# Kernel optimization log

Measured on AMD Instinct MI355X. Metric: run time of the kernel, lower is better.

Reference implementation:

```python
import jax, jax.numpy as jnp
import numpy as np

N = 50000      # nodes
E = 400000     # edges (avg degree 8)
G = 64         # graphs in batch
IN_DIM = 128
OUT_DIM = 16


def _linear_params(key, fan_in, fan_out):
    k1, k2 = jax.random.split(key)
    s = 1.0 / np.sqrt(fan_in)
    W = jax.random.uniform(k1, (fan_in, fan_out), minval=-s, maxval=s, dtype=jnp.float32)
    b = jax.random.uniform(k2, (fan_out,), minval=-s, maxval=s, dtype=jnp.float32)
    return W, b


def setup_inputs() -> dict:
    key = jax.random.key(0)
    ks = jax.random.split(key, 12)
    x = jax.random.normal(ks[0], (N, IN_DIM), dtype=jnp.float32)
    edge_index = jax.random.randint(ks[1], (2, E), 0, N)
    # balanced graph assignment (sorted, every graph id present)
    batch = (jnp.arange(N) * G) // N
    W1, b1 = _linear_params(ks[2], IN_DIM, 64)
    W2, b2 = _linear_params(ks[3], 64, 256)
    W3, b3 = _linear_params(ks[4], 256, 512)
    W4, b4 = _linear_params(ks[5], 512, 64)
    Wr, br = _linear_params(ks[6], IN_DIM, 64)
    fc1_W, fc1_b = _linear_params(ks[7], 64, 64)
    fc2_W, fc2_b = _linear_params(ks[8], 64, OUT_DIM)
    ln_g = jnp.ones((64,), jnp.float32); ln_b = jnp.zeros((64,), jnp.float32)
    fcn_g = jnp.ones((64,), jnp.float32); fcn_b = jnp.zeros((64,), jnp.float32)
    return dict(x=x, edge_index=edge_index, batch=batch,
                W1=W1, b1=b1, W2=W2, b2=b2, W3=W3, b3=b3, W4=W4, b4=b4,
                Wr=Wr, br=br, ln_g=ln_g, ln_b=ln_b,
                fc1_W=fc1_W, fc1_b=fc1_b, fcn_g=fcn_g, fcn_b=fcn_b,
                fc2_W=fc2_W, fc2_b=fc2_b)


def _leaky_relu(h):
    return jnp.where(h >= 0, h, 0.01 * h)


def _layer_norm(h, g, b, eps=1e-5):
    m = jnp.mean(h, axis=-1, keepdims=True)
    v = jnp.var(h, axis=-1, keepdims=True)
    return (h - m) * jax.lax.rsqrt(v + eps) * g + b


def reference(x, edge_index, batch, W1, b1, W2, b2, W3, b3, W4, b4,
              Wr, br, ln_g, ln_b, fc1_W, fc1_b, fcn_g, fcn_b, fc2_W, fc2_b):
    src, dst = edge_index[0], edge_index[1]
    n = x.shape[0]
    # PyG GCNConv normalization with self-loops: deg = 1 + in-degree
    deg = jax.ops.segment_sum(jnp.ones(src.shape[0], x.dtype), dst, num_segments=n) + 1.0
    dis = jax.lax.rsqrt(deg)                 # [N]
    edge_norm = (dis[src] * dis[dst])[:, None]   # [E,1]
    self_norm = (dis * dis)[:, None]             # [N,1]

    def gcn_conv(h, W, b):
        h = h @ W                                            # transform first (PyG order)
        agg = jax.ops.segment_sum(h[src] * edge_norm, dst, num_segments=n)
        return agg + h * self_norm + b                       # self-loop term + bias

    residual = x @ Wr + br
    h = _leaky_relu(gcn_conv(x, W1, b1))
    h = _leaky_relu(gcn_conv(h, W2, b2))
    h = _leaky_relu(gcn_conv(h, W3, b3))
    h = _leaky_relu(gcn_conv(h, W4, b4))
    h = _layer_norm(h + residual, ln_g, ln_b)
    # global max pool over graphs
    p = jax.ops.segment_max(h, batch, num_segments=G)        # [G,64]
    p = _layer_norm(p @ fc1_W + fc1_b, fcn_g, fcn_b)
    p = _leaky_relu(p)
    return p @ fc2_W + fc2_b                                 # [G,16]
```

## Files before the change

kernel.cpp:

```cpp
#include <hip/hip_runtime.h>
#include <hip/hip_bf16.h>
#include <math.h>

typedef short bf16x8 __attribute__((ext_vector_type(8)));
typedef short bf16x4 __attribute__((ext_vector_type(4)));
typedef float f32x4 __attribute__((ext_vector_type(4)));

__device__ inline unsigned short f2bf(float f) {
  unsigned u = __float_as_uint(f);
  u += 0x7FFF + ((u >> 16) & 1);
  return (unsigned short)(u >> 16);
}
__device__ inline float bf2f(unsigned short h) {
  return __uint_as_float(((unsigned)h) << 16);
}


__global__ __launch_bounds__(256) void zero_i32(int* __restrict__ p, int n) {
  int i = blockIdx.x * 256 + threadIdx.x;
  if (i < n) p[i] = 0;
}

__global__ __launch_bounds__(256) void count_k(const int* __restrict__ dst, int* __restrict__ cnt, int e) {
  int i = blockIdx.x * 256 + threadIdx.x;
  if (i < e) atomicAdd(&cnt[dst[i]], 1);
}

__global__ __launch_bounds__(256) void dis_k(const int* __restrict__ cnt, float* __restrict__ dis, int n) {
  int i = blockIdx.x * 256 + threadIdx.x;
  if (i < n) dis[i] = rsqrtf((float)cnt[i] + 1.0f);
}

__global__ __launch_bounds__(256) void scan_a(const int* __restrict__ cnt, int* __restrict__ bsum, int n) {
  int i = blockIdx.x * 256 + threadIdx.x;
  int v = (i < n) ? cnt[i] : 0;
#pragma unroll
  for (int o = 32; o > 0; o >>= 1) v += __shfl_xor(v, o);
  __shared__ int ws[4];
  if ((threadIdx.x & 63) == 0) ws[threadIdx.x >> 6] = v;
  __syncthreads();
  if (threadIdx.x == 0) bsum[blockIdx.x] = ws[0] + ws[1] + ws[2] + ws[3];
}

__global__ __launch_bounds__(256) void scan_b(const int* __restrict__ bsum, int* __restrict__ bpre,
                                              int* __restrict__ off_n, int nb) {
  __shared__ int s[256];
  int t = threadIdx.x;
  int v = (t < nb) ? bsum[t] : 0;
  s[t] = v;
  __syncthreads();
  for (int o = 1; o < 256; o <<= 1) {
    int u = (t >= o) ? s[t - o] : 0;
    __syncthreads();
    s[t] += u;
    __syncthreads();
  }
  if (t < nb) bpre[t] = s[t] - v;
  if (t == 255) off_n[0] = s[255];
}

__global__ __launch_bounds__(256) void scan_c(const int* __restrict__ cnt, const int* __restrict__ bpre,
                                              int* __restrict__ off, int* __restrict__ cursor, int n) {
  __shared__ int s[256];
  int i = blockIdx.x * 256 + threadIdx.x;
  int t = threadIdx.x;
  int v = (i < n) ? cnt[i] : 0;
  s[t] = v;
  __syncthreads();
  for (int o = 1; o < 256; o <<= 1) {
    int u = (t >= o) ? s[t - o] : 0;
    __syncthreads();
    s[t] += u;
    __syncthreads();
  }
  if (i < n) {
    int ov = bpre[blockIdx.x] + s[t] - v;
    off[i] = ov;
    cursor[i] = ov;
  }
}

__global__ __launch_bounds__(256) void scatter_k(const int* __restrict__ src, const int* __restrict__ dst,
                                                 int* __restrict__ cursor, int* __restrict__ csr, int e) {
  int i = blockIdx.x * 256 + threadIdx.x;
  if (i < e) {
    int p = atomicAdd(&cursor[dst[i]], 1);
    csr[p] = src[i];
  }
}


__global__ __launch_bounds__(256) void wconv_k(const float* __restrict__ W1, const float* __restrict__ Wr,
                                               const float* __restrict__ W2, const float* __restrict__ W3,
                                               const float* __restrict__ W4,
                                               short* __restrict__ o1, short* __restrict__ oR,
                                               short* __restrict__ o2, short* __restrict__ o3,
                                               short* __restrict__ o4) {
  int b = blockIdx.x;
  const float* W; short* O; int K, N, nr;
  if (b < 64)       { W = W1; O = o1; K = 128; N = 64;  nr = b; }
  else if (b < 128) { W = Wr; O = oR; K = 128; N = 64;  nr = b - 64; }
  else if (b < 384) { W = W2; O = o2; K = 64;  N = 256; nr = b - 128; }
  else if (b < 896) { W = W3; O = o3; K = 256; N = 512; nr = b - 384; }
  else              { W = W4; O = o4; K = 512; N = 64;  nr = b - 896; }
  for (int k = threadIdx.x; k < K; k += 256)
    O[(size_t)nr * K + k] = (short)f2bf(W[(size_t)k * N + nr]);
}


template<int KT, int NTOT, int WM, int WN, int BIAS, int RELU, int ABF, int OBF, int SPLIT, int SCL, int BLK>
__global__ __launch_bounds__(256, BLK) void mgemm(const void* __restrict__ Av,
                                                  const short* __restrict__ Wc,
                                                  const float* __restrict__ bias,
                                                  void* __restrict__ Cv, void* __restrict__ Cv2,
                                                  const float* __restrict__ scl, int M) {
  __shared__ short As[64 * WM][ABF ? 40 : 72];
  __shared__ short Bs[64 * WN][40];
  const int tid = threadIdx.x;
  const int row0 = blockIdx.x * (64 * WM);
  const int col0 = blockIdx.y * (64 * WN);
  const int w = tid >> 6, lane = tid & 63;
  const int wm = w / WN, wn = w % WN;
  const int rm = wm * 64, cn = wn * 64;
  const int lm = lane & 15, lk = (lane >> 4) * 8;

  f32x4 acc[4][4];
#pragma unroll
  for (int i = 0; i < 4; i++)
#pragma unroll
    for (int j = 0; j < 4; j++)
#pragma unroll
      for (int r = 0; r < 4; r++) acc[i][j][r] = 0.f;

  for (int k0 = 0; k0 < KT; k0 += 32) {
#pragma unroll
    for (int p = 0; p < WM; p++) {
      int r = (tid >> 2) + p * 64;
      int kseg = (tid & 3) * 8;
      int gr = row0 + r;
      if (ABF) {
        bf16x8 v = {0, 0, 0, 0, 0, 0, 0, 0};
        if (gr < M) v = *(const bf16x8*)((const short*)Av + (size_t)gr * KT + k0 + kseg);
        *(bf16x8*)&As[r][kseg] = v;
      } else {
        float4 v0 = {0.f, 0.f, 0.f, 0.f}, v1 = {0.f, 0.f, 0.f, 0.f};
        if (gr < M) {
          const float* ap = (const float*)Av + (size_t)gr * KT + k0 + kseg;
          v0 = *(const float4*)ap;
          v1 = *(const float4*)(ap + 4);
        }
        float vv[8] = {v0.x, v0.y, v0.z, v0.w, v1.x, v1.y, v1.z, v1.w};
        bf16x8 hv, lv;
#pragma unroll
        for (int j = 0; j < 8; j++) {
          unsigned short h = f2bf(vv[j]);
          hv[j] = (short)h;
          lv[j] = (short)f2bf(vv[j] - bf2f(h));
        }
        *(bf16x8*)&As[r][kseg] = hv;
        *(bf16x8*)&As[r][32 + kseg] = lv;
      }
    }
#pragma unroll
    for (int p = 0; p < WN; p++) {
      int nr = (tid >> 2) + p * 64;
      int seg = (tid & 3) * 8;
      *(bf16x8*)&Bs[nr][seg] = *(const bf16x8*)(Wc + (size_t)(col0 + nr) * KT + k0 + seg);
    }
    __syncthreads();

    bf16x8 ah[4], al[4], bb[4];
#pragma unroll
    for (int mt = 0; mt < 4; mt++) {
      ah[mt] = *(const bf16x8*)&As[rm + mt * 16 + lm][lk];
      if (!ABF) al[mt] = *(const bf16x8*)&As[rm + mt * 16 + lm][32 + lk];
    }
#pragma unroll
    for (int nt = 0; nt < 4; nt++) bb[nt] = *(const bf16x8*)&Bs[cn + nt * 16 + lm][lk];
#pragma unroll
    for (int mt = 0; mt < 4; mt++)
#pragma unroll
      for (int nt = 0; nt < 4; nt++) {
        acc[mt][nt] = __builtin_amdgcn_mfma_f32_16x16x32_bf16(ah[mt], bb[nt], acc[mt][nt], 0, 0, 0);
        if (!ABF)
          acc[mt][nt] = __builtin_amdgcn_mfma_f32_16x16x32_bf16(al[mt], bb[nt], acc[mt][nt], 0, 0, 0);
      }
    __syncthreads();
  }

  if (SPLIT) {
    float* O = (wn == 0) ? (float*)Cv : (float*)Cv2;
#pragma unroll
    for (int mt = 0; mt < 4; mt++) {
      int grb = row0 + rm + mt * 16 + (lane >> 4) * 4;
#pragma unroll
      for (int nt = 0; nt < 4; nt++) {
        int gc = nt * 16 + lm;
        float bv = (wn == 1) ? bias[gc] : 0.f;
#pragma unroll
        for (int r = 0; r < 4; r++) {
          int gr = grb + r;
          if (gr < M) {
            float v = acc[mt][nt][r];
            if (wn == 0 && SCL) v *= scl[gr];
            else v += bv;
            O[(size_t)gr * 64 + gc] = v;
          }
        }
      }
    }
  } else if (OBF && WM == 1) {
    short* epi = &Bs[0][0];
    const int NCOL = 64 * WN;
    float bvv[4];
#pragma unroll
    for (int nt = 0; nt < 4; nt++) bvv[nt] = BIAS ? bias[col0 + cn + nt * 16 + lm] : 0.f;
#pragma unroll
    for (int mt = 0; mt < 4; mt++) {
      __syncthreads();
#pragma unroll
      for (int r = 0; r < 4; r++) {
        int gr = row0 + mt * 16 + (lane >> 4) * 4 + r;
        float sc = (SCL && gr < M) ? scl[gr] : 1.f;
#pragma unroll
        for (int nt = 0; nt < 4; nt++) {
          float v = acc[mt][nt][r] + bvv[nt];
          if (RELU) v = (v >= 0.f) ? v : 0.01f * v;
          if (SCL) v *= sc;
          epi[((lane >> 4) * 4 + r) * NCOL + cn + nt * 16 + lm] = (short)f2bf(v);
        }
      }
      __syncthreads();
      const int per = (16 * NCOL) / 256;
      int base = tid * per;
      int lr = base / NCOL, lc = base % NCOL;
      int gr = row0 + mt * 16 + lr;
      if (gr < M) {
#pragma unroll
        for (int q = 0; q < per / 8; q++)
          *(bf16x8*)((short*)Cv + (size_t)gr * NTOT + col0 + lc + q * 8) = *(bf16x8*)&epi[base + q * 8];
      }
    }
  } else {
#pragma unroll
    for (int mt = 0; mt < 4; mt++) {
      int grb = row0 + rm + mt * 16 + (lane >> 4) * 4;
#pragma unroll
      for (int nt = 0; nt < 4; nt++) {
        int gc = col0 + cn + nt * 16 + lm;
        float bv = BIAS ? bias[gc] : 0.f;
#pragma unroll
        for (int r = 0; r < 4; r++) {
          int gr = grb + r;
          if (gr < M) {
            float v = acc[mt][nt][r] + bv;
            if (RELU) v = (v >= 0.f) ? v : 0.01f * v;
            if (SCL) v *= scl[gr];
            if (OBF) ((short*)Cv)[(size_t)gr * NTOT + gc] = (short)f2bf(v);
            else     ((float*)Cv)[(size_t)gr * NTOT + gc] = v;
          }
        }
      }
    }
  }
}


__global__ __launch_bounds__(256, 3) void fused34_k(const short* __restrict__ z3,
                                                    const short* __restrict__ W3c,
                                                    const float* __restrict__ b3,
                                                    const short* __restrict__ W4c,
                                                    const float* __restrict__ dis,
                                                    float* __restrict__ T4, int M) {
  __shared__ short Bs[64][264];
  __shared__ short Hs[64][72];
  __shared__ short Ws4[64][72];
  const int tid = threadIdx.x;
  const int row0 = blockIdx.x * 64;
  const int w = tid >> 6, lane = tid & 63;
  const int lm = lane & 15, lk = (lane >> 4) * 8;
  const int rquad = (lane >> 4) * 4;
  const int srow = tid >> 2, sseg = (tid & 3) * 8;

  bf16x8 afr[8];
  {
    int gr = row0 + w * 16 + lm;
    bool ok = gr < M;
    const short* zp = z3 + (size_t)gr * 256 + lk;
#pragma unroll
    for (int kc = 0; kc < 8; kc++) {
      bf16x8 v = {0, 0, 0, 0, 0, 0, 0, 0};
      if (ok) v = *(const bf16x8*)(zp + kc * 32);
      afr[kc] = v;
    }
  }

  f32x4 t4acc[4];
#pragma unroll
  for (int nt = 0; nt < 4; nt++)
#pragma unroll
    for (int r = 0; r < 4; r++) t4acc[nt][r] = 0.f;

  for (int c = 0; c < 8; c++) {
#pragma unroll
    for (int q = 0; q < 8; q++) {
      int flat = q * 2048 + tid * 8;
      int rr = flat >> 8, cc = flat & 255;
      *(bf16x8*)&Bs[rr][cc] = *(const bf16x8*)(W3c + (size_t)c * 64 * 256 + flat);
    }
    *(bf16x8*)&Ws4[srow][sseg]      = *(const bf16x8*)(W4c + (size_t)srow * 512 + c * 64 + sseg);
    *(bf16x8*)&Ws4[srow][32 + sseg] = *(const bf16x8*)(W4c + (size_t)srow * 512 + c * 64 + 32 + sseg);
    __syncthreads();

    f32x4 acc1[4];
#pragma unroll
    for (int nt = 0; nt < 4; nt++)
#pragma unroll
      for (int r = 0; r < 4; r++) acc1[nt][r] = 0.f;
#pragma unroll
    for (int k0 = 0; k0 < 8; k0++) {
      bf16x8 bb[4];
#pragma unroll
      for (int nt = 0; nt < 4; nt++) bb[nt] = *(const bf16x8*)&Bs[nt * 16 + lm][k0 * 32 + lk];
#pragma unroll
      for (int nt = 0; nt < 4; nt++)
        acc1[nt] = __builtin_amdgcn_mfma_f32_16x16x32_bf16(afr[k0], bb[nt], acc1[nt], 0, 0, 0);
    }
#pragma unroll
    for (int nt = 0; nt < 4; nt++) {
      float bv = b3[c * 64 + nt * 16 + lm];
#pragma unroll
      for (int r = 0; r < 4; r++) {
        float v = acc1[nt][r] + bv;
        v = (v >= 0.f) ? v : 0.01f * v;
        Hs[w * 16 + rquad + r][nt * 16 + lm] = (short)f2bf(v);
      }
    }
#pragma unroll
    for (int kk = 0; kk < 64; kk += 32) {
      bf16x8 ah2 = *(const bf16x8*)&Hs[w * 16 + lm][kk + lk];
      bf16x8 bb2[4];
#pragma unroll
      for (int nt = 0; nt < 4; nt++) bb2[nt] = *(const bf16x8*)&Ws4[nt * 16 + lm][kk + lk];
#pragma unroll
      for (int nt = 0; nt < 4; nt++)
        t4acc[nt] = __builtin_amdgcn_mfma_f32_16x16x32_bf16(ah2, bb2[nt], t4acc[nt], 0, 0, 0);
    }
    __syncthreads();
  }
#pragma unroll
  for (int r = 0; r < 4; r++) {
    int gr = row0 + w * 16 + rquad + r;
    float sc = (gr < M) ? dis[gr] : 0.f;
#pragma unroll
    for (int nt = 0; nt < 4; nt++) {
      int gc = nt * 16 + lm;
      if (gr < M) T4[(size_t)gr * 64 + gc] = t4acc[nt][r] * sc;
    }
  }
}


template<int BR, int OSCL>
__global__ __launch_bounds__(256) void agg64_k(const float* __restrict__ T, const float* __restrict__ dis,
                                               const int* __restrict__ off, const int* __restrict__ csr,
                                               const float* __restrict__ bias, float* __restrict__ Out, int n) {
  int wid = (blockIdx.x * 256 + threadIdx.x) >> 6;
  int lane = threadIdx.x & 63;
  if (wid >= n) return;
  float di = dis[wid];
  int e0 = off[wid], e1 = off[wid + 1];
  float acc = T[(size_t)wid * 64 + lane];
  int e = e0;
  for (; e + 4 <= e1; e += 4) {
    int j0 = csr[e], j1 = csr[e + 1], j2 = csr[e + 2], j3 = csr[e + 3];
    float v0 = T[(size_t)j0 * 64 + lane];
    float v1 = T[(size_t)j1 * 64 + lane];
    float v2 = T[(size_t)j2 * 64 + lane];
    float v3 = T[(size_t)j3 * 64 + lane];
    acc += (v0 + v1) + (v2 + v3);
  }
  for (; e < e1; e++) acc += T[(size_t)csr[e] * 64 + lane];
  float v = di * acc;
  if (BR) {
    v += bias[lane];
    v = (v >= 0.f) ? v : 0.01f * v;
  }
  if (OSCL) v *= di;
  Out[(size_t)wid * 64 + lane] = v;
}

__global__ __launch_bounds__(256) void agg64_ln_k(const float* __restrict__ T, const float* __restrict__ dis,
                                                  const int* __restrict__ off, const int* __restrict__ csr,
                                                  const float* __restrict__ bias, const float* __restrict__ resid,
                                                  const float* __restrict__ g, const float* __restrict__ b,
                                                  float* __restrict__ outh, int n) {
  int wid = (blockIdx.x * 256 + threadIdx.x) >> 6;
  int lane = threadIdx.x & 63;
  if (wid >= n) return;
  float di = dis[wid];
  int e0 = off[wid], e1 = off[wid + 1];
  float acc = T[(size_t)wid * 64 + lane];
  int e = e0;
  for (; e + 4 <= e1; e += 4) {
    int j0 = csr[e], j1 = csr[e + 1], j2 = csr[e + 2], j3 = csr[e + 3];
    float v0 = T[(size_t)j0 * 64 + lane];
    float v1 = T[(size_t)j1 * 64 + lane];
    float v2 = T[(size_t)j2 * 64 + lane];
    float v3 = T[(size_t)j3 * 64 + lane];
    acc += (v0 + v1) + (v2 + v3);
  }
  for (; e < e1; e++) acc += T[(size_t)csr[e] * 64 + lane];
  float v = di * acc + bias[lane];
  v = (v >= 0.f) ? v : 0.01f * v;
  v += resid[(size_t)wid * 64 + lane];
  float s = v, ss = v * v;
#pragma unroll
  for (int o = 32; o > 0; o >>= 1) {
    s += __shfl_xor(s, o);
    ss += __shfl_xor(ss, o);
  }
  float m = s * (1.f / 64.f);
  float var = ss * (1.f / 64.f) - m * m;
  float y = (v - m) * rsqrtf(var + 1e-5f) * g[lane] + b[lane];
  outh[(size_t)wid * 64 + lane] = y;
}

__global__ __launch_bounds__(256) void agg256b_k(const short* __restrict__ T, const float* __restrict__ dis,
                                                 const int* __restrict__ off, const int* __restrict__ csr,
                                                 short* __restrict__ Out, int n) {
  int wid = (blockIdx.x * 256 + threadIdx.x) >> 6;
  int lane = threadIdx.x & 63;
  if (wid >= n) return;
  float di = dis[wid];
  int e0 = off[wid], e1 = off[wid + 1];
  bf16x4 sf = *(const bf16x4*)&T[(size_t)wid * 256 + lane * 4];
  float a0 = bf2f((unsigned short)sf[0]);
  float a1 = bf2f((unsigned short)sf[1]);
  float a2 = bf2f((unsigned short)sf[2]);
  float a3 = bf2f((unsigned short)sf[3]);
  int e = e0;
  for (; e + 4 <= e1; e += 4) {
    int j0 = csr[e], j1 = csr[e + 1], j2 = csr[e + 2], j3 = csr[e + 3];
    bf16x4 t0 = *(const bf16x4*)&T[(size_t)j0 * 256 + lane * 4];
    bf16x4 t1 = *(const bf16x4*)&T[(size_t)j1 * 256 + lane * 4];
    bf16x4 t2 = *(const bf16x4*)&T[(size_t)j2 * 256 + lane * 4];
    bf16x4 t3 = *(const bf16x4*)&T[(size_t)j3 * 256 + lane * 4];
    a0 += (bf2f((unsigned short)t0[0]) + bf2f((unsigned short)t1[0])) +
          (bf2f((unsigned short)t2[0]) + bf2f((unsigned short)t3[0]));
    a1 += (bf2f((unsigned short)t0[1]) + bf2f((unsigned short)t1[1])) +
          (bf2f((unsigned short)t2[1]) + bf2f((unsigned short)t3[1]));
    a2 += (bf2f((unsigned short)t0[2]) + bf2f((unsigned short)t1[2])) +
          (bf2f((unsigned short)t2[2]) + bf2f((unsigned short)t3[2]));
    a3 += (bf2f((unsigned short)t0[3]) + bf2f((unsigned short)t1[3])) +
          (bf2f((unsigned short)t2[3]) + bf2f((unsigned short)t3[3]));
  }
  for (; e < e1; e++) {
    bf16x4 t = *(const bf16x4*)&T[(size_t)csr[e] * 256 + lane * 4];
    a0 += bf2f((unsigned short)t[0]);
    a1 += bf2f((unsigned short)t[1]);
    a2 += bf2f((unsigned short)t[2]);
    a3 += bf2f((unsigned short)t[3]);
  }
  bf16x4 o;
  o[0] = (short)f2bf(di * a0);
  o[1] = (short)f2bf(di * a1);
  o[2] = (short)f2bf(di * a2);
  o[3] = (short)f2bf(di * a3);
  *(bf16x4*)&Out[(size_t)wid * 256 + lane * 4] = o;
}


__global__ __launch_bounds__(256) void pool_k(const float* __restrict__ hn, float* __restrict__ p, int n) {
  const int G = 64;
  int g = blockIdx.x;
  int f = threadIdx.x & 63, c = threadIdx.x >> 6;
  long long s = ((long long)g * n + G - 1) / G;
  long long e = ((long long)(g + 1) * n + G - 1) / G;
  float m = -INFINITY;
  for (long long i = s + c; i < e; i += 4) m = fmaxf(m, hn[(size_t)i * 64 + f]);
  __shared__ float red[4][64];
  red[c][f] = m;
  __syncthreads();
  if (c == 0) {
    m = fmaxf(fmaxf(red[0][f], red[1][f]), fmaxf(red[2][f], red[3][f]));
    p[g * 64 + f] = m;
  }
}


__global__ __launch_bounds__(64) void mlp_k(const float* __restrict__ p, const float* __restrict__ fc1W,
                                            const float* __restrict__ fc1b, const float* __restrict__ fng,
                                            const float* __restrict__ fnb, const float* __restrict__ fc2W,
                                            const float* __restrict__ fc2b, float* __restrict__ out) {
  int g = blockIdx.x;
  int lane = threadIdx.x;
  __shared__ float ps[64], qs[64];
  ps[lane] = p[g * 64 + lane];
  __syncthreads();
  float q = fc1b[lane];
#pragma unroll 8
  for (int k = 0; k < 64; k++) q = fmaf(ps[k], fc1W[k * 64 + lane], q);
  float s = q, ss = q * q;
#pragma unroll
  for (int o = 32; o > 0; o >>= 1) {
    s += __shfl_xor(s, o);
    ss += __shfl_xor(ss, o);
  }
  float m = s * (1.f / 64.f);
  float var = ss * (1.f / 64.f) - m * m;
  float y = (q - m) * rsqrtf(var + 1e-5f) * fng[lane] + fnb[lane];
  y = (y >= 0.f) ? y : 0.01f * y;
  qs[lane] = y;
  __syncthreads();
  if (lane < 16) {
    float o = fc2b[lane];
#pragma unroll 8
    for (int k = 0; k < 64; k++) o = fmaf(qs[k], fc2W[k * 16 + lane], o);
    out[g * 16 + lane] = o;
  }
}


extern "C" void kernel_launch(void* const* d_in, const int* in_sizes, int n_in,
                              void* d_out, int out_size, void* d_ws, size_t ws_size,
                              hipStream_t stream) {
  const float* x   = (const float*)d_in[0];
  const int*   ei  = (const int*)d_in[1];
  const float* W1  = (const float*)d_in[3];
  const float* b1  = (const float*)d_in[4];
  const float* W2  = (const float*)d_in[5];
  const float* b2  = (const float*)d_in[6];
  const float* W3  = (const float*)d_in[7];
  const float* b3  = (const float*)d_in[8];
  const float* W4  = (const float*)d_in[9];
  const float* b4  = (const float*)d_in[10];
  const float* Wr  = (const float*)d_in[11];
  const float* br  = (const float*)d_in[12];
  const float* lng = (const float*)d_in[13];
  const float* lnb = (const float*)d_in[14];
  const float* f1W = (const float*)d_in[15];
  const float* f1b = (const float*)d_in[16];
  const float* fng = (const float*)d_in[17];
  const float* fnb = (const float*)d_in[18];
  const float* f2W = (const float*)d_in[19];
  const float* f2b = (const float*)d_in[20];

  int n = in_sizes[0] / 128;
  int e = in_sizes[1] / 2;
  const int* src = ei;
  const int* dst = ei + e;

  float* arena = (float*)d_ws;
  float* resid = arena;
  short* h2b   = (short*)(arena + (size_t)64 * n);
  float* t4    = arena + (size_t)64 * n;
  short* z3b   = (short*)(arena + (size_t)192 * n);
  float* hn    = arena + (size_t)192 * n;
  float* z2    = arena + (size_t)256 * n;
  float* h1    = arena + (size_t)320 * n;
  float* t1    = arena + (size_t)384 * n;
  float* dis   = arena + (size_t)448 * n;
  int* cnt    = (int*)(dis + n);
  int* off    = cnt + n;
  int* cursor = off + n + 1;
  int* csr    = cursor + n;
  int* bsum   = csr + e;
  int* bpre   = bsum + 256;
  float* pool = (float*)(bpre + 256);
  size_t wq = (((size_t)(pool + 4096)) + 15) & ~(size_t)15;
  short* wc1 = (short*)wq;
  short* wcR = wc1 + 8192;
  short* wc2 = wcR + 8192;
  short* wc3 = wc2 + 16384;
  short* wc4 = wc3 + 131072;
  size_t need = ((char*)(wc4 + 32768) - (char*)d_ws) + 64;
  if (ws_size < need) return;

  int nb_n = (n + 255) / 256;
  int nb_e = (e + 255) / 256;
  int nb_w = (n + 3) / 4;
  int g_wide = (n + 63) / 64;
  int g_fused = (n + 127) / 128;

  wconv_k<<<960, 256, 0, stream>>>(W1, Wr, W2, W3, W4, wc1, wcR, wc2, wc3, wc4);

  zero_i32<<<nb_n, 256, 0, stream>>>(cnt, n);
  count_k<<<nb_e, 256, 0, stream>>>(dst, cnt, e);
  dis_k<<<nb_n, 256, 0, stream>>>(cnt, dis, n);
  scan_a<<<nb_n, 256, 0, stream>>>(cnt, bsum, n);
  scan_b<<<1, 256, 0, stream>>>(bsum, bpre, off + n, nb_n);
  scan_c<<<nb_n, 256, 0, stream>>>(cnt, bpre, off, cursor, n);
  scatter_k<<<nb_e, 256, 0, stream>>>(src, dst, cursor, csr, e);

  mgemm<128, 128, 2, 2, 1, 0, 0, 0, 1, 1, 4><<<dim3(g_fused, 1), 256, 0, stream>>>(x, wc1, br, t1, resid, dis, n);
  agg64_k<1, 1><<<nb_w, 256, 0, stream>>>(t1, dis, off, csr, b1, h1, n);
  agg64_k<0, 0><<<nb_w, 256, 0, stream>>>(h1, dis, off, csr, nullptr, z2, n);
  mgemm<64, 256, 1, 4, 1, 1, 0, 1, 0, 1, 5><<<dim3(g_wide, 1), 256, 0, stream>>>(z2, wc2, b2, h2b, nullptr, dis, n);
  agg256b_k<<<nb_w, 256, 0, stream>>>(h2b, dis, off, csr, z3b, n);
  fused34_k<<<g_wide, 256, 0, stream>>>(z3b, wc3, b3, wc4, dis, t4, n);
  agg64_ln_k<<<nb_w, 256, 0, stream>>>(t4, dis, off, csr, b4, resid, lng, lnb, hn, n);
  pool_k<<<64, 256, 0, stream>>>(hn, pool, n);
  mlp_k<<<64, 64, 0, stream>>>(pool, f1W, f1b, fng, fnb, f2W, f2b, (float*)d_out);
}
```

Measured before the change: 397.7 us.

## Store layer-1/2 intermediates in bf16 and shrink fused34 tiles for occupancy

The first GEMM's split epilogue now writes the scaled transform as bf16, staged through shared memory for coalesced 16-byte stores. The two 64-wide aggregation kernels then read and write bf16 instead of fp32, and the second GEMM takes bf16 input. This roughly halves the gather traffic of those passes. Separately, fused34_k processes 32-column chunks of W3 with smaller LDS buffers and raises its launch-bounds occupancy target from 3 to 5, at the cost of more loop iterations and barriers, plus some loss of precision in the intermediates.

```diff
diff --git a/kernel.cpp b/kernel.cpp
--- a/kernel.cpp
+++ b/kernel.cpp
@@ -189,25 +189,44 @@
   }
 
   if (SPLIT) {
-    float* O = (wn == 0) ? (float*)Cv : (float*)Cv2;
-#pragma unroll
-    for (int mt = 0; mt < 4; mt++) {
-      int grb = row0 + rm + mt * 16 + (lane >> 4) * 4;
-#pragma unroll
-      for (int nt = 0; nt < 4; nt++) {
-        int gc = nt * 16 + lm;
-        float bv = (wn == 1) ? bias[gc] : 0.f;
+    short* epi = (short*)&As[0][0];
+    if (wn == 0) {
+#pragma unroll
+      for (int mt = 0; mt < 4; mt++) {
+        int lr = rm + mt * 16 + (lane >> 4) * 4;
 #pragma unroll
         for (int r = 0; r < 4; r++) {
-          int gr = grb + r;
-          if (gr < M) {
-            float v = acc[mt][nt][r];
-            if (wn == 0 && SCL) v *= scl[gr];
-            else v += bv;
-            O[(size_t)gr * 64 + gc] = v;
+          int gr = row0 + lr + r;
+          float sc = (SCL && gr < M) ? scl[gr] : 0.f;
+#pragma unroll
+          for (int nt = 0; nt < 4; nt++)
+            epi[(lr + r) * 64 + nt * 16 + lm] = (short)f2bf(acc[mt][nt][r] * sc);
+        }
+      }
+    } else {
+#pragma unroll
+      for (int mt = 0; mt < 4; mt++) {
+        int grb = row0 + rm + mt * 16 + (lane >> 4) * 4;
+#pragma unroll
+        for (int nt = 0; nt < 4; nt++) {
+          int gc = nt * 16 + lm;
+          float bv = bias[gc];
+#pragma unroll
+          for (int r = 0; r < 4; r++) {
+            int gr = grb + r;
+            if (gr < M) ((float*)Cv2)[(size_t)gr * 64 + gc] = acc[mt][nt][r] + bv;
           }
         }
       }
+    }
+    __syncthreads();
+    int base = tid * 32;
+    int row = base >> 6, col = base & 63;
+    int gr = row0 + row;
+    if (gr < M) {
+#pragma unroll
+      for (int q = 0; q < 4; q++)
+        *(bf16x8*)((short*)Cv + (size_t)gr * 64 + col + q * 8) = *(bf16x8*)&epi[base + q * 8];
     }
   } else if (OBF && WM == 1) {
     short* epi = &Bs[0][0];
@@ -266,21 +285,20 @@
 }
 
 
-__global__ __launch_bounds__(256, 3) void fused34_k(const short* __restrict__ z3,
+__global__ __launch_bounds__(256, 5) void fused34_k(const short* __restrict__ z3,
                                                     const short* __restrict__ W3c,
                                                     const float* __restrict__ b3,
                                                     const short* __restrict__ W4c,
                                                     const float* __restrict__ dis,
                                                     float* __restrict__ T4, int M) {
-  __shared__ short Bs[64][264];
-  __shared__ short Hs[64][72];
-  __shared__ short Ws4[64][72];
+  __shared__ short Bs[32][264];
+  __shared__ short Hs[64][40];
+  __shared__ short Ws4[64][40];
   const int tid = threadIdx.x;
   const int row0 = blockIdx.x * 64;
   const int w = tid >> 6, lane = tid & 63;
   const int lm = lane & 15, lk = (lane >> 4) * 8;
   const int rquad = (lane >> 4) * 4;
-  const int srow = tid >> 2, sseg = (tid & 3) * 8;
 
   bf16x8 afr[8];
   {
@@ -301,34 +319,35 @@
 #pragma unroll
     for (int r = 0; r < 4; r++) t4acc[nt][r] = 0.f;
 
-  for (int c = 0; c < 8; c++) {
-#pragma unroll
-    for (int q = 0; q < 8; q++) {
+  for (int c = 0; c < 16; c++) {
+#pragma unroll
+    for (int q = 0; q < 4; q++) {
       int flat = q * 2048 + tid * 8;
       int rr = flat >> 8, cc = flat & 255;
-      *(bf16x8*)&Bs[rr][cc] = *(const bf16x8*)(W3c + (size_t)c * 64 * 256 + flat);
-    }
-    *(bf16x8*)&Ws4[srow][sseg]      = *(const bf16x8*)(W4c + (size_t)srow * 512 + c * 64 + sseg);
-    *(bf16x8*)&Ws4[srow][32 + sseg] = *(const bf16x8*)(W4c + (size_t)srow * 512 + c * 64 + 32 + sseg);
-    __syncthreads();
-
-    f32x4 acc1[4];
-#pragma unroll
-    for (int nt = 0; nt < 4; nt++)
+      *(bf16x8*)&Bs[rr][cc] = *(const bf16x8*)(W3c + (size_t)c * 32 * 256 + flat);
+    }
+    Ws4[tid >> 2][(tid & 3) * 8 + 0] = 0;
+    *(bf16x8*)&Ws4[tid >> 2][(tid & 3) * 8] =
+        *(const bf16x8*)(W4c + (size_t)(tid >> 2) * 512 + c * 32 + (tid & 3) * 8);
+    __syncthreads();
+
+    f32x4 acc1[2];
+#pragma unroll
+    for (int nt = 0; nt < 2; nt++)
 #pragma unroll
       for (int r = 0; r < 4; r++) acc1[nt][r] = 0.f;
 #pragma unroll
     for (int k0 = 0; k0 < 8; k0++) {
-      bf16x8 bb[4];
-#pragma unroll
-      for (int nt = 0; nt < 4; nt++) bb[nt] = *(const bf16x8*)&Bs[nt * 16 + lm][k0 * 32 + lk];
-#pragma unroll
-      for (int nt = 0; nt < 4; nt++)
+      bf16x8 bb[2];
+#pragma unroll
+      for (int nt = 0; nt < 2; nt++) bb[nt] = *(const bf16x8*)&Bs[nt * 16 + lm][k0 * 32 + lk];
+#pragma unroll
+      for (int nt = 0; nt < 2; nt++)
         acc1[nt] = __builtin_amdgcn_mfma_f32_16x16x32_bf16(afr[k0], bb[nt], acc1[nt], 0, 0, 0);
     }
 #pragma unroll
-    for (int nt = 0; nt < 4; nt++) {
-      float bv = b3[c * 64 + nt * 16 + lm];
+    for (int nt = 0; nt < 2; nt++) {
+      float bv = b3[c * 32 + nt * 16 + lm];
 #pragma unroll
       for (int r = 0; r < 4; r++) {
         float v = acc1[nt][r] + bv;
@@ -336,12 +355,11 @@
         Hs[w * 16 + rquad + r][nt * 16 + lm] = (short)f2bf(v);
       }
     }
-#pragma unroll
-    for (int kk = 0; kk < 64; kk += 32) {
-      bf16x8 ah2 = *(const bf16x8*)&Hs[w * 16 + lm][kk + lk];
+    {
+      bf16x8 ah2 = *(const bf16x8*)&Hs[w * 16 + lm][lk];
       bf16x8 bb2[4];
 #pragma unroll
-      for (int nt = 0; nt < 4; nt++) bb2[nt] = *(const bf16x8*)&Ws4[nt * 16 + lm][kk + lk];
+      for (int nt = 0; nt < 4; nt++) bb2[nt] = *(const bf16x8*)&Ws4[nt * 16 + lm][lk];
 #pragma unroll
       for (int nt = 0; nt < 4; nt++)
         t4acc[nt] = __builtin_amdgcn_mfma_f32_16x16x32_bf16(ah2, bb2[nt], t4acc[nt], 0, 0, 0);
@@ -362,32 +380,32 @@
 
 
 template<int BR, int OSCL>
-__global__ __launch_bounds__(256) void agg64_k(const float* __restrict__ T, const float* __restrict__ dis,
-                                               const int* __restrict__ off, const int* __restrict__ csr,
-                                               const float* __restrict__ bias, float* __restrict__ Out, int n) {
+__global__ __launch_bounds__(256) void aggb64_k(const short* __restrict__ T, const float* __restrict__ dis,
+                                                const int* __restrict__ off, const int* __restrict__ csr,
+                                                const float* __restrict__ bias, short* __restrict__ Out, int n) {
   int wid = (blockIdx.x * 256 + threadIdx.x) >> 6;
   int lane = threadIdx.x & 63;
   if (wid >= n) return;
   float di = dis[wid];
   int e0 = off[wid], e1 = off[wid + 1];
-  float acc = T[(size_t)wid * 64 + lane];
+  float acc = bf2f((unsigned short)T[(size_t)wid * 64 + lane]);
   int e = e0;
   for (; e + 4 <= e1; e += 4) {
     int j0 = csr[e], j1 = csr[e + 1], j2 = csr[e + 2], j3 = csr[e + 3];
-    float v0 = T[(size_t)j0 * 64 + lane];
-    float v1 = T[(size_t)j1 * 64 + lane];
-    float v2 = T[(size_t)j2 * 64 + lane];
-    float v3 = T[(size_t)j3 * 64 + lane];
+    float v0 = bf2f((unsigned short)T[(size_t)j0 * 64 + lane]);
+    float v1 = bf2f((unsigned short)T[(size_t)j1 * 64 + lane]);
+    float v2 = bf2f((unsigned short)T[(size_t)j2 * 64 + lane]);
+    float v3 = bf2f((unsigned short)T[(size_t)j3 * 64 + lane]);
     acc += (v0 + v1) + (v2 + v3);
   }
-  for (; e < e1; e++) acc += T[(size_t)csr[e] * 64 + lane];
+  for (; e < e1; e++) acc += bf2f((unsigned short)T[(size_t)csr[e] * 64 + lane]);
   float v = di * acc;
   if (BR) {
     v += bias[lane];
     v = (v >= 0.f) ? v : 0.01f * v;
   }
   if (OSCL) v *= di;
-  Out[(size_t)wid * 64 + lane] = v;
+  Out[(size_t)wid * 64 + lane] = (short)f2bf(v);
 }
 
 __global__ __launch_bounds__(256) void agg64_ln_k(const float* __restrict__ T, const float* __restrict__ dis,
@@ -557,9 +575,9 @@
   float* t4    = arena + (size_t)64 * n;
   short* z3b   = (short*)(arena + (size_t)192 * n);
   float* hn    = arena + (size_t)192 * n;
-  float* z2    = arena + (size_t)256 * n;
-  float* h1    = arena + (size_t)320 * n;
-  float* t1    = arena + (size_t)384 * n;
+  short* t1b   = (short*)(arena + (size_t)320 * n);
+  short* h1b   = (short*)(arena + (size_t)352 * n);
+  short* z2b   = (short*)(arena + (size_t)384 * n);
   float* dis   = arena + (size_t)448 * n;
   int* cnt    = (int*)(dis + n);
   int* off    = cnt + n;
@@ -593,10 +611,10 @@
   scan_c<<<nb_n, 256, 0, stream>>>(cnt, bpre, off, cursor, n);
   scatter_k<<<nb_e, 256, 0, stream>>>(src, dst, cursor, csr, e);
 
-  mgemm<128, 128, 2, 2, 1, 0, 0, 0, 1, 1, 4><<<dim3(g_fused, 1), 256, 0, stream>>>(x, wc1, br, t1, resid, dis, n);
-  agg64_k<1, 1><<<nb_w, 256, 0, stream>>>(t1, dis, off, csr, b1, h1, n);
-  agg64_k<0, 0><<<nb_w, 256, 0, stream>>>(h1, dis, off, csr, nullptr, z2, n);
-  mgemm<64, 256, 1, 4, 1, 1, 0, 1, 0, 1, 5><<<dim3(g_wide, 1), 256, 0, stream>>>(z2, wc2, b2, h2b, nullptr, dis, n);
+  mgemm<128, 128, 2, 2, 1, 0, 0, 0, 1, 1, 4><<<dim3(g_fused, 1), 256, 0, stream>>>(x, wc1, br, t1b, resid, dis, n);
+  aggb64_k<1, 1><<<nb_w, 256, 0, stream>>>(t1b, dis, off, csr, b1, h1b, n);
+  aggb64_k<0, 0><<<nb_w, 256, 0, stream>>>(h1b, dis, off, csr, nullptr, z2b, n);
+  mgemm<64, 256, 1, 4, 1, 1, 1, 1, 0, 1, 5><<<dim3(g_wide, 1), 256, 0, stream>>>(z2b, wc2, b2, h2b, nullptr, dis, n);
   agg256b_k<<<nb_w, 256, 0, stream>>>(h2b, dis, off, csr, z3b, n);
   fused34_k<<<g_wide, 256, 0, stream>>>(z3b, wc3, b3, wc4, dis, t4, n);
   agg64_ln_k<<<nb_w, 256, 0, stream>>>(t4, dis, off, csr, b4, resid, lng, lnb, hn, n);
```

Result: faster. 387.9 us (-2.5%).
